# Performance work log

Measured on AMD Instinct MI355X. Metric: run time of the kernel, lower is better.

The kernel has to match this reference:

```python
import jax, jax.numpy as jnp
import numpy as np

N = 100000
E = 800000
DIMS = [128, 128, 128, 256, 256]  # layer in/out widths
NUM_CLASSES = 4


def _xavier(key, shape, gain):
    fan_in, fan_out = shape[0], shape[1]
    bound = gain * np.sqrt(6.0 / (fan_in + fan_out))
    return jax.random.uniform(key, shape, jnp.float32, -bound, bound)


def setup_inputs() -> dict:
    key = jax.random.key(0)
    ks = jax.random.split(key, 8)
    gain = np.sqrt(2.0)  # calculate_gain('relu')
    inp = {
        "x": jax.random.normal(ks[0], (N, DIMS[0]), jnp.float32),
        "src": jax.random.randint(ks[1], (E,), 0, N, jnp.int32),
        "dst": jax.random.randint(ks[2], (E,), 0, N, jnp.int32),
    }
    for i in range(4):
        inp[f"W{i}"] = _xavier(ks[3 + i], (DIMS[i], DIMS[i + 1]), gain)
        inp[f"b{i}"] = jnp.zeros((DIMS[i + 1],), jnp.float32)
    inp["Wc"] = _xavier(ks[7], (DIMS[4], NUM_CLASSES), gain)
    inp["bc"] = jnp.zeros((NUM_CLASSES,), jnp.float32)
    return inp


def _graph_conv(x, W, b, src, dst, norm_src, norm_dst):
    # DGL GraphConv, norm='both': scale by out-deg^-1/2, W, SpMM (sum over
    # edges src->dst), scale by in-deg^-1/2, +bias, ReLU. (A(XW)=(AX)W so
    # weight-order branch in DGL is math-equivalent.)
    h = (x * norm_src) @ W                      # [N, out]
    agg = jax.ops.segment_sum(h[src], dst, num_segments=x.shape[0])
    return jax.nn.relu(agg * norm_dst + b)


def reference(x, src, dst, W0, b0, W1, b1, W2, b2, W3, b3, Wc, bc):
    ones = jnp.ones((src.shape[0],), jnp.float32)
    deg_out = jnp.clip(jax.ops.segment_sum(ones, src, num_segments=N), 1.0)
    deg_in = jnp.clip(jax.ops.segment_sum(ones, dst, num_segments=N), 1.0)
    norm_src = (deg_out ** -0.5)[:, None]
    norm_dst = (deg_in ** -0.5)[:, None]
    h = x
    for W, b in ((W0, b0), (W1, b1), (W2, b2), (W3, b3)):
        h = _graph_conv(h, W, b, src, dst, norm_src, norm_dst)
        # dropout(p=0.5) is identity in eval mode
    return h @ Wc + bc
```

## Files before the change

### kernel.cpp

```cpp
#include <hip/hip_runtime.h>
#include <cstdint>
#include <cstddef>

#define NN 100000
#define NEDGE 800000
#define NBUCK 196
#define RNG 512

typedef __attribute__((ext_vector_type(8))) short short8v;
typedef __attribute__((ext_vector_type(16))) float float16v;

__device__ inline ushort f2bf(float f) {
    uint32_t u = __float_as_uint(f);
    u += 0x7fff + ((u >> 16) & 1);
    return (ushort)(u >> 16);
}
__device__ inline float bf2f(ushort h) { return __uint_as_float(((uint32_t)h) << 16); }
__device__ inline void split2(float a, ushort& h, ushort& l) {
    h = f2bf(a);
    l = f2bf(a - bf2f(h));
}

__device__ inline void gload16(const void* g, void* lds) {
    __builtin_amdgcn_global_load_lds(
        (const __attribute__((address_space(1))) void*)g,
        (__attribute__((address_space(3))) void*)lds, 16, 0, 0);
}


__global__ __launch_bounds__(256) void binA(const int* __restrict__ src, const int* __restrict__ dst,
                                            int* __restrict__ dstBinCnt, int* __restrict__ srcBinCnt, int E) {
    __shared__ int hd[NBUCK], hs[NBUCK];
    for (int i = threadIdx.x; i < NBUCK; i += 256) { hd[i] = 0; hs[i] = 0; }
    __syncthreads();
    for (int i = blockIdx.x * 256 + threadIdx.x; i < E; i += gridDim.x * 256) {
        atomicAdd(&hs[src[i] >> 9], 1);
        atomicAdd(&hd[dst[i] >> 9], 1);
    }
    __syncthreads();
    for (int i = threadIdx.x; i < NBUCK; i += 256) {
        if (hd[i]) atomicAdd(&dstBinCnt[i], hd[i]);
        if (hs[i]) atomicAdd(&srcBinCnt[i], hs[i]);
    }
}

__global__ void binScan(const int* __restrict__ dstBinCnt, const int* __restrict__ srcBinCnt,
                        int* __restrict__ dstBase, int* __restrict__ srcBase,
                        int* __restrict__ dstCur, int* __restrict__ srcCur) {
    if (threadIdx.x == 0 && blockIdx.x == 0) {
        int a = 0;
        for (int i = 0; i < NBUCK; i++) { dstBase[i] = a; dstCur[i] = a; a += dstBinCnt[i]; }
        dstBase[NBUCK] = a;
        a = 0;
        for (int i = 0; i < NBUCK; i++) { srcBase[i] = a; srcCur[i] = a; a += srcBinCnt[i]; }
        srcBase[NBUCK] = a;
    }
}

__global__ __launch_bounds__(256) void partition_kernel(
        const int* __restrict__ src, const int* __restrict__ dst,
        int* __restrict__ dstCur, int* __restrict__ srcCur,
        int2* __restrict__ pairBuck, int* __restrict__ srcBuck, int E) {
    __shared__ int cd[NBUCK], bd[NBUCK], cs[NBUCK], bs[NBUCK];
    const int CH = (E + gridDim.x - 1) / gridDim.x;
    const int lo = blockIdx.x * CH;
    const int hi = min(lo + CH, E);
    for (int i = threadIdx.x; i < NBUCK; i += 256) { cd[i] = 0; cs[i] = 0; }
    __syncthreads();
    for (int i = lo + threadIdx.x; i < hi; i += 256) {
        atomicAdd(&cd[dst[i] >> 9], 1);
        atomicAdd(&cs[src[i] >> 9], 1);
    }
    __syncthreads();
    for (int i = threadIdx.x; i < NBUCK; i += 256) {
        bd[i] = cd[i] ? atomicAdd(&dstCur[i], cd[i]) : 0;
        bs[i] = cs[i] ? atomicAdd(&srcCur[i], cs[i]) : 0;
        cd[i] = 0; cs[i] = 0;
    }
    __syncthreads();
    for (int i = lo + threadIdx.x; i < hi; i += 256) {
        int s = src[i], d = dst[i];
        int slot = atomicAdd(&cd[d >> 9], 1);
        pairBuck[bd[d >> 9] + slot] = make_int2(s, d);
        int slot2 = atomicAdd(&cs[s >> 9], 1);
        srcBuck[bs[s >> 9] + slot2] = s;
    }
}

__global__ __launch_bounds__(256) void srcHist(const int* __restrict__ srcBuck,
                                               const int* __restrict__ srcBase,
                                               float* __restrict__ ns, int n) {
    __shared__ int h[RNG];
    const int k = blockIdx.x;
    for (int i = threadIdx.x; i < RNG; i += 256) h[i] = 0;
    __syncthreads();
    const int lo = srcBase[k], hi = srcBase[k + 1];
    for (int i = lo + threadIdx.x; i < hi; i += 256)
        atomicAdd(&h[srcBuck[i] & (RNG - 1)], 1);
    __syncthreads();
    for (int i = threadIdx.x; i < RNG; i += 256) {
        int idx = k * RNG + i;
        if (idx < n) ns[idx] = 1.0f / sqrtf((float)max(h[i], 1));
    }
}

__global__ __launch_bounds__(256) void dstBuild(const int2* __restrict__ pairBuck,
                                                const int* __restrict__ dstBase,
                                                float* __restrict__ nd, int* __restrict__ rowptr,
                                                int* __restrict__ permSrc, int n) {
    __shared__ int h[RNG];
    __shared__ int tsum[256];
    const int k = blockIdx.x;
    const int t = threadIdx.x;
    for (int i = t; i < RNG; i += 256) h[i] = 0;
    __syncthreads();
    const int lo = dstBase[k], hi = dstBase[k + 1];
    for (int i = lo + t; i < hi; i += 256)
        atomicAdd(&h[pairBuck[i].y & (RNG - 1)], 1);
    __syncthreads();
    int a0 = h[2 * t], a1 = h[2 * t + 1];
    tsum[t] = a0 + a1;
    __syncthreads();
    for (int off = 1; off < 256; off <<= 1) {
        int v = (t >= off) ? tsum[t - off] : 0;
        __syncthreads();
        tsum[t] += v;
        __syncthreads();
    }
    const int pre = lo + (t > 0 ? tsum[t - 1] : 0);
    const int r0 = pre, r1 = pre + a0;
    const int idx0 = k * RNG + 2 * t;
    if (idx0 <= n) rowptr[idx0] = r0;
    if (idx0 + 1 <= n) rowptr[idx0 + 1] = r1;
    if (idx0 < n) nd[idx0] = 1.0f / sqrtf((float)max(a0, 1));
    if (idx0 + 1 < n) nd[idx0 + 1] = 1.0f / sqrtf((float)max(a1, 1));
    h[2 * t] = r0;
    h[2 * t + 1] = r1;
    __syncthreads();
    for (int i = lo + t; i < hi; i += 256) {
        int2 p = pairBuck[i];
        int pos = atomicAdd(&h[p.y & (RNG - 1)], 1);
        permSrc[pos] = p.x;
    }
}


__global__ void convx_kernel(const float* __restrict__ x, const float* __restrict__ ns,
                             ushort* __restrict__ actB, int n) {
    int idx = blockIdx.x * blockDim.x + threadIdx.x;
    if (idx >= n * 32) return;
    int node = idx >> 5;
    int f0 = (idx & 31) * 4;
    float sc = ns[node];
    float4 v = *reinterpret_cast<const float4*>(x + (size_t)node * 128 + f0);
    ushort4 h;
    h.x = f2bf(v.x * sc);
    h.y = f2bf(v.y * sc);
    h.z = f2bf(v.z * sc);
    h.w = f2bf(v.w * sc);
    *reinterpret_cast<ushort4*>(actB + (size_t)node * 128 + f0) = h;
}

__global__ void convw_all(const float* __restrict__ W0, const float* __restrict__ W1,
                          const float* __restrict__ W2, const float* __restrict__ W3,
                          ushort* __restrict__ Wth, ushort* __restrict__ Wtl) {
    int idx = blockIdx.x * blockDim.x + threadIdx.x;
    if (idx >= 131072) return;
    const float* W; int K, logD, base;
    if (idx < 16384)      { W = W0; K = 128; logD = 7; base = 0; }
    else if (idx < 32768) { W = W1; K = 128; logD = 7; base = 16384; }
    else if (idx < 65536) { W = W2; K = 128; logD = 8; base = 32768; }
    else                  { W = W3; K = 256; logD = 8; base = 65536; }
    int loc = idx - base;
    int k = loc >> logD, d = loc & ((1 << logD) - 1);
    ushort h, l;
    split2(W[loc], h, l);
    Wth[base + d * K + k] = h;
    Wtl[base + d * K + k] = l;
}


__device__ inline void accum8(float* a, uint4 v) {
    a[0] += __uint_as_float(v.x << 16);
    a[1] += __uint_as_float(v.x & 0xffff0000u);
    a[2] += __uint_as_float(v.y << 16);
    a[3] += __uint_as_float(v.y & 0xffff0000u);
    a[4] += __uint_as_float(v.z << 16);
    a[5] += __uint_as_float(v.z & 0xffff0000u);
    a[6] += __uint_as_float(v.w << 16);
    a[7] += __uint_as_float(v.w & 0xffff0000u);
}

template<int D>
__global__ __launch_bounds__(256) void agg_kernel(
        const ushort* __restrict__ act, const int* __restrict__ rowptr,
        const int* __restrict__ permSrc, const float* __restrict__ nd,
        ushort* __restrict__ Rb, int n) {
    int node = blockIdx.x * 4 + (threadIdx.x >> 6);
    if (node >= n) return;
    int lane = threadIdx.x & 63;
    constexpr int GROUPS = (D == 256) ? 2 : 4;
    constexpr int GL = 64 / GROUPS;
    const int g  = lane / GL;
    const int gl = lane % GL;
    const int f0 = gl * 8;
    float a[8] = {0.f,0.f,0.f,0.f,0.f,0.f,0.f,0.f};
    int r0 = rowptr[node], r1 = rowptr[node + 1];

    int e = r0 + g;
    for (; e + 3 * GROUPS < r1; e += 4 * GROUPS) {
        int s0 = permSrc[e];
        int s1 = permSrc[e + GROUPS];
        int s2 = permSrc[e + 2 * GROUPS];
        int s3 = permSrc[e + 3 * GROUPS];
        uint4 v0 = *reinterpret_cast<const uint4*>(act + (size_t)s0 * D + f0);
        uint4 v1 = *reinterpret_cast<const uint4*>(act + (size_t)s1 * D + f0);
        uint4 v2 = *reinterpret_cast<const uint4*>(act + (size_t)s2 * D + f0);
        uint4 v3 = *reinterpret_cast<const uint4*>(act + (size_t)s3 * D + f0);
        accum8(a, v0); accum8(a, v1); accum8(a, v2); accum8(a, v3);
    }
    for (; e < r1; e += GROUPS) {
        int s = permSrc[e];
        accum8(a, *reinterpret_cast<const uint4*>(act + (size_t)s * D + f0));
    }

    #pragma unroll
    for (int j = 0; j < 8; j++) {
        if constexpr (GROUPS == 4) a[j] += __shfl_xor(a[j], 16);
        a[j] += __shfl_xor(a[j], 32);
    }

    if (g == 0) {
        float sc = nd[node];
        union { ushort u[8]; uint4 v; } H;
        #pragma unroll
        for (int j = 0; j < 8; j++) H.u[j] = f2bf(a[j] * sc);
        *reinterpret_cast<uint4*>(Rb + (size_t)node * D + f0) = H.v;
    }
}


__global__ __launch_bounds__(256) void gemm_mfma(
        const ushort* __restrict__ A,
        const ushort* __restrict__ Bhi, const ushort* __restrict__ Blo,
        const float* __restrict__ bias, const float* __restrict__ post,
        ushort* __restrict__ Cb, int n, int K, int Dout, int logCB, int nrowp) {
    __shared__ __align__(16) ushort sA[128][64];
    __shared__ __align__(16) ushort sBh[64][64];
    __shared__ __align__(16) ushort sBl[64][64];
    const int tid = threadIdx.x;
    const int lane = tid & 63;
    const int wid = tid >> 6;
    const int l31 = lane & 31;
    const int kg = lane >> 5;

    const int bid = blockIdx.x;
    const int xcd = bid & 7;
    const int t = bid >> 3;
    const int cb2 = t & ((1 << logCB) - 1);
    const int rp = (t >> logCB) * 8 + xcd;
    if (rp >= nrowp) return;
    const int row0 = rp * 128;
    const int col0 = cb2 * 64;

    const ushort* gA[4];
    char* lA[4];
    #pragma unroll
    for (int i = 0; i < 4; i++) {
        int slot = i * 256 + wid * 64 + lane;
        int r = slot >> 3, ch = slot & 7;
        int gch = ch ^ (r & 7);
        int row = row0 + r; if (row >= n) row = n - 1;
        gA[i] = A + (size_t)row * K + gch * 8;
        lA[i] = (char*)&sA[0][0] + (size_t)(i * 256 + wid * 64) * 16;
    }
    const ushort* gBh[2]; const ushort* gBl[2];
    char* lB[2];
    #pragma unroll
    for (int i = 0; i < 2; i++) {
        int slot = i * 256 + wid * 64 + lane;
        int r = slot >> 3, ch = slot & 7;
        int gch = ch ^ (r & 7);
        gBh[i] = Bhi + (size_t)(col0 + r) * K + gch * 8;
        gBl[i] = Blo + (size_t)(col0 + r) * K + gch * 8;
        lB[i] = (char*)&sBh[0][0] + (size_t)(i * 256 + wid * 64) * 16;
    }
    const size_t lblo = (char*)&sBl[0][0] - (char*)&sBh[0][0];

    float16v acc0 = {0.f,0.f,0.f,0.f,0.f,0.f,0.f,0.f,0.f,0.f,0.f,0.f,0.f,0.f,0.f,0.f};
    float16v acc1 = {0.f,0.f,0.f,0.f,0.f,0.f,0.f,0.f,0.f,0.f,0.f,0.f,0.f,0.f,0.f,0.f};

    for (int k0 = 0; k0 < K; k0 += 64) {
        #pragma unroll
        for (int i = 0; i < 4; i++) gload16(gA[i] + k0, lA[i]);
        #pragma unroll
        for (int i = 0; i < 2; i++) {
            gload16(gBh[i] + k0, lB[i]);
            gload16(gBl[i] + k0, lB[i] + lblo);
        }
        __syncthreads();

        #pragma unroll
        for (int ks = 0; ks < 4; ks++) {
            const int gw = ks * 2 + kg;
            const int rA = wid * 32 + l31;
            const int rB0 = l31, rB1 = 32 + l31;
            short8v a = *reinterpret_cast<const short8v*>(&sA[rA][(gw ^ (rA & 7)) * 8]);
            short8v bh0 = *reinterpret_cast<const short8v*>(&sBh[rB0][(gw ^ (rB0 & 7)) * 8]);
            short8v bl0 = *reinterpret_cast<const short8v*>(&sBl[rB0][(gw ^ (rB0 & 7)) * 8]);
            short8v bh1 = *reinterpret_cast<const short8v*>(&sBh[rB1][(gw ^ (rB1 & 7)) * 8]);
            short8v bl1 = *reinterpret_cast<const short8v*>(&sBl[rB1][(gw ^ (rB1 & 7)) * 8]);
            acc0 = __builtin_amdgcn_mfma_f32_32x32x16_bf16(a, bh0, acc0, 0, 0, 0);
            acc1 = __builtin_amdgcn_mfma_f32_32x32x16_bf16(a, bh1, acc1, 0, 0, 0);
            acc0 = __builtin_amdgcn_mfma_f32_32x32x16_bf16(a, bl0, acc0, 0, 0, 0);
            acc1 = __builtin_amdgcn_mfma_f32_32x32x16_bf16(a, bl1, acc1, 0, 0, 0);
        }
        __syncthreads();
    }

    const int rbase = row0 + wid * 32;
    #pragma unroll
    for (int cb = 0; cb < 2; cb++) {
        const int colg = col0 + cb * 32 + l31;
        const float bcol = bias[colg];
        const float16v& acc = cb ? acc1 : acc0;
        #pragma unroll
        for (int r = 0; r < 16; r++) {
            int rowg = rbase + (r & 3) + 8 * (r >> 2) + 4 * kg;
            if (rowg < n) {
                float v = fmaxf(acc[r] + bcol, 0.0f);
                if (post) v *= post[rowg];
                Cb[(size_t)rowg * Dout + colg] = f2bf(v);
            }
        }
    }
}


__global__ __launch_bounds__(256) void classifier_kernel(
        const ushort* __restrict__ h, const float* __restrict__ Wc,
        const float* __restrict__ bc, float* __restrict__ out, int n) {
    __shared__ float Ws[256 * 4];
    int tid = threadIdx.x;
    for (int i = tid; i < 1024; i += 256) Ws[i] = Wc[i];
    __syncthreads();
    int node = blockIdx.x * 64 + (tid >> 2);
    int c = tid & 3;
    if (node < n) {
        float sum = bc[c];
        const ushort* hr = h + (size_t)node * 256;
        #pragma unroll
        for (int k0 = 0; k0 < 256; k0 += 8) {
            uint4 pk = *reinterpret_cast<const uint4*>(hr + k0);
            sum = fmaf(bf2f((ushort)(pk.x & 0xffff)), Ws[(k0 + 0) * 4 + c], sum);
            sum = fmaf(bf2f((ushort)(pk.x >> 16)),    Ws[(k0 + 1) * 4 + c], sum);
            sum = fmaf(bf2f((ushort)(pk.y & 0xffff)), Ws[(k0 + 2) * 4 + c], sum);
            sum = fmaf(bf2f((ushort)(pk.y >> 16)),    Ws[(k0 + 3) * 4 + c], sum);
            sum = fmaf(bf2f((ushort)(pk.z & 0xffff)), Ws[(k0 + 4) * 4 + c], sum);
            sum = fmaf(bf2f((ushort)(pk.z >> 16)),    Ws[(k0 + 5) * 4 + c], sum);
            sum = fmaf(bf2f((ushort)(pk.w & 0xffff)), Ws[(k0 + 6) * 4 + c], sum);
            sum = fmaf(bf2f((ushort)(pk.w >> 16)),    Ws[(k0 + 7) * 4 + c], sum);
        }
        out[(size_t)node * 4 + c] = sum;
    }
}


extern "C" void kernel_launch(void* const* d_in, const int* in_sizes, int n_in,
                              void* d_out, int out_size, void* d_ws, size_t ws_size,
                              hipStream_t stream) {
    const float* x   = (const float*)d_in[0];
    const int*   src = (const int*)d_in[1];
    const int*   dst = (const int*)d_in[2];
    const float* W0 = (const float*)d_in[3];
    const float* b0 = (const float*)d_in[4];
    const float* W1 = (const float*)d_in[5];
    const float* b1 = (const float*)d_in[6];
    const float* W2 = (const float*)d_in[7];
    const float* b2 = (const float*)d_in[8];
    const float* W3 = (const float*)d_in[9];
    const float* b3 = (const float*)d_in[10];
    const float* Wc = (const float*)d_in[11];
    const float* bc = (const float*)d_in[12];
    const float* b[4] = {b0, b1, b2, b3};
    float* out = (float*)d_out;

    ushort* actB = (ushort*)d_ws;
    ushort* Rb   = actB + (size_t)NN * 256;
    float*  ns   = (float*)(Rb + (size_t)NN * 256);
    float*  nd   = ns + NN;
    ushort* Wth  = (ushort*)(nd + NN);
    ushort* Wtl  = Wth + 131072;
    int*    rowptr  = (int*)(Wtl + 131072);
    int*    permSrc = rowptr + (NN + 1);
    int*    dstBinCnt = permSrc + NEDGE;
    int*    srcBinCnt = dstBinCnt + NBUCK;
    int*    dstBase   = srcBinCnt + NBUCK;
    int*    srcBase   = dstBase + NBUCK + 1;
    int*    dstCur    = srcBase + NBUCK + 1;
    int*    srcCur    = dstCur + NBUCK;
    int2*   pairBuck = (int2*)Rb;
    int*    srcBuck  = (int*)(pairBuck + NEDGE);
    (void)in_sizes; (void)n_in; (void)out_size; (void)ws_size;

    hipMemsetAsync(dstBinCnt, 0, 2 * NBUCK * sizeof(int), stream);
    binA<<<256, 256, 0, stream>>>(src, dst, dstBinCnt, srcBinCnt, NEDGE);
    binScan<<<1, 64, 0, stream>>>(dstBinCnt, srcBinCnt, dstBase, srcBase, dstCur, srcCur);
    partition_kernel<<<256, 256, 0, stream>>>(src, dst, dstCur, srcCur, pairBuck, srcBuck, NEDGE);
    convw_all<<<512, 256, 0, stream>>>(W0, W1, W2, W3, Wth, Wtl);
    srcHist<<<NBUCK, 256, 0, stream>>>(srcBuck, srcBase, ns, NN);
    dstBuild<<<NBUCK, 256, 0, stream>>>(pairBuck, dstBase, nd, rowptr, permSrc, NN);

    convx_kernel<<<(NN * 32 + 255) / 256, 256, 0, stream>>>(x, ns, actB, NN);

    const int dims[5] = {128, 128, 128, 256, 256};
    const int woff[4] = {0, 16384, 32768, 65536};
    const int nrowp = (NN + 127) / 128;
    const int nrowp8 = ((nrowp + 7) / 8) * 8;

    for (int l = 0; l < 4; l++) {
        int K = dims[l], Dout = dims[l + 1];
        int logCB = (Dout == 128) ? 1 : 2;
        int CB = Dout / 64;

        int ablocks = (NN + 3) / 4;
        if (K == 128)
            agg_kernel<128><<<ablocks, 256, 0, stream>>>(actB, rowptr, permSrc, nd, Rb, NN);
        else
            agg_kernel<256><<<ablocks, 256, 0, stream>>>(actB, rowptr, permSrc, nd, Rb, NN);

        const float* post = (l < 3) ? ns : nullptr;
        gemm_mfma<<<nrowp8 * CB, 256, 0, stream>>>(Rb, Wth + woff[l], Wtl + woff[l], b[l], post,
                                                   actB, NN, K, Dout, logCB, nrowp);
    }

    classifier_kernel<<<(NN + 63) / 64, 256, 0, stream>>>(actB, Wc, bc, out, NN);
}
```

Before: 457.4 us.

## Drop bf16 hi/lo weight split and sort CSR neighbor lists

Weights are now converted to a single bf16 array instead of a hi/lo pair, which halves the MFMA count and the B-tile loads and LDS in the GEMM. This lowers weight precision and may loosen accuracy against the fp32 reference. It also adds a per-row insertion sort of permSrc inside dstBuild, making the neighbor order deterministic and ascending so gathers in aggregation may have better locality. The sort adds serial per-thread work to graph construction.

After: 475.1 us. 1.04x slower.

```diff
diff --git a/kernel.cpp b/kernel.cpp
--- a/kernel.cpp
+++ b/kernel.cpp
@@ -16,10 +16,6 @@
     return (ushort)(u >> 16);
 }
 __device__ inline float bf2f(ushort h) { return __uint_as_float(((uint32_t)h) << 16); }
-__device__ inline void split2(float a, ushort& h, ushort& l) {
-    h = f2bf(a);
-    l = f2bf(a - bf2f(h));
-}
 
 __device__ inline void gload16(const void* g, void* lds) {
     __builtin_amdgcn_global_load_lds(
@@ -141,6 +137,21 @@
         int2 p = pairBuck[i];
         int pos = atomicAdd(&h[p.y & (RNG - 1)], 1);
         permSrc[pos] = p.x;
+    }
+    __syncthreads();
+    if (idx0 < n) {
+        for (int i = r0 + 1; i < r0 + a0; i++) {
+            int v = permSrc[i]; int j = i - 1;
+            while (j >= r0 && permSrc[j] > v) { permSrc[j + 1] = permSrc[j]; j--; }
+            permSrc[j + 1] = v;
+        }
+    }
+    if (idx0 + 1 < n) {
+        for (int i = r1 + 1; i < r1 + a1; i++) {
+            int v = permSrc[i]; int j = i - 1;
+            while (j >= r1 && permSrc[j] > v) { permSrc[j + 1] = permSrc[j]; j--; }
+            permSrc[j + 1] = v;
+        }
     }
 }
 
@@ -163,7 +174,7 @@
 
 __global__ void convw_all(const float* __restrict__ W0, const float* __restrict__ W1,
                           const float* __restrict__ W2, const float* __restrict__ W3,
-                          ushort* __restrict__ Wth, ushort* __restrict__ Wtl) {
+                          ushort* __restrict__ Wt) {
     int idx = blockIdx.x * blockDim.x + threadIdx.x;
     if (idx >= 131072) return;
     const float* W; int K, logD, base;
@@ -173,10 +184,7 @@
     else                  { W = W3; K = 256; logD = 8; base = 65536; }
     int loc = idx - base;
     int k = loc >> logD, d = loc & ((1 << logD) - 1);
-    ushort h, l;
-    split2(W[loc], h, l);
-    Wth[base + d * K + k] = h;
-    Wtl[base + d * K + k] = l;
+    Wt[base + d * K + k] = f2bf(W[loc]);
 }
 
 
@@ -241,13 +249,11 @@
 
 
 __global__ __launch_bounds__(256) void gemm_mfma(
-        const ushort* __restrict__ A,
-        const ushort* __restrict__ Bhi, const ushort* __restrict__ Blo,
+        const ushort* __restrict__ A, const ushort* __restrict__ B,
         const float* __restrict__ bias, const float* __restrict__ post,
         ushort* __restrict__ Cb, int n, int K, int Dout, int logCB, int nrowp) {
     __shared__ __align__(16) ushort sA[128][64];
-    __shared__ __align__(16) ushort sBh[64][64];
-    __shared__ __align__(16) ushort sBl[64][64];
+    __shared__ __align__(16) ushort sB[64][64];
     const int tid = threadIdx.x;
     const int lane = tid & 63;
     const int wid = tid >> 6;
@@ -274,18 +280,16 @@
         gA[i] = A + (size_t)row * K + gch * 8;
         lA[i] = (char*)&sA[0][0] + (size_t)(i * 256 + wid * 64) * 16;
     }
-    const ushort* gBh[2]; const ushort* gBl[2];
+    const ushort* gB[2];
     char* lB[2];
     #pragma unroll
     for (int i = 0; i < 2; i++) {
         int slot = i * 256 + wid * 64 + lane;
         int r = slot >> 3, ch = slot & 7;
         int gch = ch ^ (r & 7);
-        gBh[i] = Bhi + (size_t)(col0 + r) * K + gch * 8;
-        gBl[i] = Blo + (size_t)(col0 + r) * K + gch * 8;
-        lB[i] = (char*)&sBh[0][0] + (size_t)(i * 256 + wid * 64) * 16;
-    }
-    const size_t lblo = (char*)&sBl[0][0] - (char*)&sBh[0][0];
+        gB[i] = B + (size_t)(col0 + r) * K + gch * 8;
+        lB[i] = (char*)&sB[0][0] + (size_t)(i * 256 + wid * 64) * 16;
+    }
 
     float16v acc0 = {0.f,0.f,0.f,0.f,0.f,0.f,0.f,0.f,0.f,0.f,0.f,0.f,0.f,0.f,0.f,0.f};
     float16v acc1 = {0.f,0.f,0.f,0.f,0.f,0.f,0.f,0.f,0.f,0.f,0.f,0.f,0.f,0.f,0.f,0.f};
@@ -294,10 +298,7 @@
         #pragma unroll
         for (int i = 0; i < 4; i++) gload16(gA[i] + k0, lA[i]);
         #pragma unroll
-        for (int i = 0; i < 2; i++) {
-            gload16(gBh[i] + k0, lB[i]);
-            gload16(gBl[i] + k0, lB[i] + lblo);
-        }
+        for (int i = 0; i < 2; i++) gload16(gB[i] + k0, lB[i]);
         __syncthreads();
 
         #pragma unroll
@@ -306,14 +307,10 @@
             const int rA = wid * 32 + l31;
             const int rB0 = l31, rB1 = 32 + l31;
             short8v a = *reinterpret_cast<const short8v*>(&sA[rA][(gw ^ (rA & 7)) * 8]);
-            short8v bh0 = *reinterpret_cast<const short8v*>(&sBh[rB0][(gw ^ (rB0 & 7)) * 8]);
-            short8v bl0 = *reinterpret_cast<const short8v*>(&sBl[rB0][(gw ^ (rB0 & 7)) * 8]);
-            short8v bh1 = *reinterpret_cast<const short8v*>(&sBh[rB1][(gw ^ (rB1 & 7)) * 8]);
-            short8v bl1 = *reinterpret_cast<const short8v*>(&sBl[rB1][(gw ^ (rB1 & 7)) * 8]);
-            acc0 = __builtin_amdgcn_mfma_f32_32x32x16_bf16(a, bh0, acc0, 0, 0, 0);
-            acc1 = __builtin_amdgcn_mfma_f32_32x32x16_bf16(a, bh1, acc1, 0, 0, 0);
-            acc0 = __builtin_amdgcn_mfma_f32_32x32x16_bf16(a, bl0, acc0, 0, 0, 0);
-            acc1 = __builtin_amdgcn_mfma_f32_32x32x16_bf16(a, bl1, acc1, 0, 0, 0);
+            short8v b0 = *reinterpret_cast<const short8v*>(&sB[rB0][(gw ^ (rB0 & 7)) * 8]);
+            short8v b1 = *reinterpret_cast<const short8v*>(&sB[rB1][(gw ^ (rB1 & 7)) * 8]);
+            acc0 = __builtin_amdgcn_mfma_f32_32x32x16_bf16(a, b0, acc0, 0, 0, 0);
+            acc1 = __builtin_amdgcn_mfma_f32_32x32x16_bf16(a, b1, acc1, 0, 0, 0);
         }
         __syncthreads();
     }
@@ -389,9 +386,8 @@
     ushort* Rb   = actB + (size_t)NN * 256;
     float*  ns   = (float*)(Rb + (size_t)NN * 256);
     float*  nd   = ns + NN;
-    ushort* Wth  = (ushort*)(nd + NN);
-    ushort* Wtl  = Wth + 131072;
-    int*    rowptr  = (int*)(Wtl + 131072);
+    ushort* Wt   = (ushort*)(nd + NN);
+    int*    rowptr  = (int*)(Wt + 131072);
     int*    permSrc = rowptr + (NN + 1);
     int*    dstBinCnt = permSrc + NEDGE;
     int*    srcBinCnt = dstBinCnt + NBUCK;
@@ -407,7 +403,7 @@
     binA<<<256, 256, 0, stream>>>(src, dst, dstBinCnt, srcBinCnt, NEDGE);
     binScan<<<1, 64, 0, stream>>>(dstBinCnt, srcBinCnt, dstBase, srcBase, dstCur, srcCur);
     partition_kernel<<<256, 256, 0, stream>>>(src, dst, dstCur, srcCur, pairBuck, srcBuck, NEDGE);
-    convw_all<<<512, 256, 0, stream>>>(W0, W1, W2, W3, Wth, Wtl);
+    convw_all<<<512, 256, 0, stream>>>(W0, W1, W2, W3, Wt);
     srcHist<<<NBUCK, 256, 0, stream>>>(srcBuck, srcBase, ns, NN);
     dstBuild<<<NBUCK, 256, 0, stream>>>(pairBuck, dstBase, nd, rowptr, permSrc, NN);
 
@@ -430,7 +426,7 @@
             agg_kernel<256><<<ablocks, 256, 0, stream>>>(actB, rowptr, permSrc, nd, Rb, NN);
 
         const float* post = (l < 3) ? ns : nullptr;
-        gemm_mfma<<<nrowp8 * CB, 256, 0, stream>>>(Rb, Wth + woff[l], Wtl + woff[l], b[l], post,
+        gemm_mfma<<<nrowp8 * CB, 256, 0, stream>>>(Rb, Wt + woff[l], b[l], post,
                                                    actB, NN, K, Dout, logCB, nrowp);
     }
 
```
